# Performance work log

Hardware: AMD Instinct MI355X
Metric: run time of the kernel (lower is better)

Reference implementation:

```python
import jax, jax.numpy as jnp
import numpy as np

N_EMBD = 1024
N_HEAD = 16
B, T = 8, 1024

def setup_inputs() -> dict:
    key = jax.random.key(0)
    ks = jax.random.split(key, 5)
    s = 0.02
    return {
        'x': jax.random.normal(ks[0], (B, T, N_EMBD), dtype=jnp.float32),
        'w_attn': jax.random.normal(ks[1], (N_EMBD, 3 * N_EMBD), dtype=jnp.float32) * s,
        'b_attn': jax.random.normal(ks[2], (3 * N_EMBD,), dtype=jnp.float32) * s,
        'w_proj': jax.random.normal(ks[3], (N_EMBD, N_EMBD), dtype=jnp.float32) * s,
        'b_proj': jax.random.normal(ks[4], (N_EMBD,), dtype=jnp.float32) * s,
    }

def reference(x, w_attn, b_attn, w_proj, b_proj):
    Bb, Tt, C = x.shape
    hd = C // N_HEAD  # head dim
    qkv = x @ w_attn + b_attn                      # [B,T,3C]
    q, k, v = jnp.split(qkv, 3, axis=2)
    # [B,T,C] -> [B,H,T,hd]
    def to_heads(t):
        return t.reshape(Bb, Tt, N_HEAD, hd).transpose(0, 2, 1, 3)
    q, k, v = to_heads(q), to_heads(k), to_heads(v)
    scale = 1.0 / jnp.sqrt(jnp.asarray(hd, dtype=x.dtype))
    att = jnp.einsum('bhqd,bhkd->bhqk', q, k) * scale  # [B,H,T,T]
    causal = jnp.tril(jnp.ones((Tt, Tt), dtype=bool))  # [T,T]
    att = jnp.where(causal[None, None, :, :], att, -jnp.inf)
    att = jax.nn.softmax(att, axis=-1)
    y = jnp.einsum('bhqk,bhkd->bhqd', att, v)          # [B,H,T,hd]
    y = y.transpose(0, 2, 1, 3).reshape(Bb, Tt, C)
    y = y @ w_proj + b_proj
    return y
```

## Files before the change

### kernel.cpp

```cpp
#include <hip/hip_runtime.h>
#include <stdint.h>

#define N_EMBD 1024
#define NHEAD  16
#define HDIM   64
#define BATCH  8
#define SEQ    1024
#define MROWS  (BATCH*SEQ)

typedef __bf16 bf16x8 __attribute__((ext_vector_type(8)));
typedef float  f32x4  __attribute__((ext_vector_type(4)));

__device__ inline unsigned short f2bf(float f) {
  uint32_t u = __float_as_uint(f);
  u += 0x7FFFu + ((u >> 16) & 1u);
  return (unsigned short)(u >> 16);
}

__device__ inline f32x4 mfma_bf16(bf16x8 a, bf16x8 b, f32x4 c) {
  return __builtin_amdgcn_mfma_f32_16x16x32_bf16(a, b, c, 0, 0, 0);
}

__device__ inline void gload_lds16(const unsigned short* g, unsigned short* l) {
  __builtin_amdgcn_global_load_lds(
      (const __attribute__((address_space(1))) void*)g,
      (__attribute__((address_space(3))) void*)l,
      16, 0, 0);
}

#define DSB __builtin_amdgcn_sched_barrier(0)
#define BARRIER __builtin_amdgcn_s_barrier()
#define VMC(n) asm volatile("s_waitcnt vmcnt(" #n ")" ::: "memory")
#define LGKM0 asm volatile("s_waitcnt lgkmcnt(0)" ::: "memory"); DSB

__global__ __launch_bounds__(256) void prep_kernel(
    const float* __restrict__ x, unsigned short* __restrict__ xb,
    const float* __restrict__ wa, unsigned short* __restrict__ oa,
    const float* __restrict__ wp, unsigned short* __restrict__ op) {
  int bid = blockIdx.x;
  int t = threadIdx.x;
  if (bid < 8192) {
    int i = (bid * 256 + t) * 4;
    float4 v = *(const float4*)(x + i);
    ushort4 o;
    o.x = f2bf(v.x); o.y = f2bf(v.y); o.z = f2bf(v.z); o.w = f2bf(v.w);
    *(ushort4*)(xb + i) = o;
    return;
  }
  __shared__ unsigned short tile[64 * 72];
  int idx = bid - 8192;
  int bx = idx & 63;
  int ky = idx >> 6;
  const int K = 1024;
  const float* in; unsigned short* out; int N;
  if (bx < 48) { in = wa; out = oa; N = 3072; }
  else         { in = wp; out = op; N = 1024; bx -= 48; }
  int k0 = ky * 64, n0 = bx * 64;
  {
    int col = (t & 15) * 4;
#pragma unroll
    for (int it = 0; it < 4; ++it) {
      int row = (t >> 4) + it * 16;
      float4 v = *(const float4*)(in + (size_t)(k0 + row) * N + n0 + col);
      ushort4 o;
      o.x = f2bf(v.x); o.y = f2bf(v.y); o.z = f2bf(v.z); o.w = f2bf(v.w);
      *(ushort4*)&tile[row * 72 + col] = o;
    }
  }
  __syncthreads();
  {
    int kcol = (t & 7) * 8;
#pragma unroll
    for (int it = 0; it < 2; ++it) {
      int nrow = (t >> 3) + it * 32;
      alignas(16) unsigned short tmp[8];
#pragma unroll
      for (int j = 0; j < 8; ++j) tmp[j] = tile[(kcol + j) * 72 + nrow];
      *(uint4*)(out + (size_t)(n0 + nrow) * K + k0 + kcol) = *(const uint4*)tmp;
    }
  }
}

__global__ __launch_bounds__(256, 3) void gemm_qkv(
    const unsigned short* __restrict__ A, const unsigned short* __restrict__ Bt,
    const float* __restrict__ bias,
    unsigned short* __restrict__ Qo, unsigned short* __restrict__ Ko,
    unsigned short* __restrict__ VTo) {
  __shared__ unsigned short Asl[256 * 64];
  __shared__ unsigned short Bsl[128 * 64];
  const int bid = blockIdx.x;
  const int xcd = bid & 7;
  const int local = bid >> 3;
  const int nchunk = local >> 5;
  const int rem = local & 31;
  const int m0 = (xcd * 4 + (rem >> 3)) * 256;
  const int n0 = (nchunk * 8 + (rem & 7)) * 128;
  const int tid = threadIdx.x;
  const int l = tid & 63, w = tid >> 6;
  const int wr = w >> 1, wc = w & 1;
  const int g = l >> 4, fr = l & 15;
  f32x4 acc[8][4];
#pragma unroll
  for (int i = 0; i < 8; ++i)
#pragma unroll
    for (int j = 0; j < 4; ++j)
#pragma unroll
      for (int r = 0; r < 4; ++r) acc[i][j][r] = 0.0f;
  const int rr = tid >> 3;
  const int cs = ((tid & 7) * 16) ^ ((rr & 7) << 4);
  const char* srcA[8];
  const char* srcB[4];
#pragma unroll
  for (int c = 0; c < 8; ++c)
    srcA[c] = (const char*)A + (size_t)(m0 + c * 32 + rr) * 2048 + cs;
#pragma unroll
  for (int c = 0; c < 4; ++c)
    srcB[c] = (const char*)Bt + (size_t)(n0 + c * 32 + rr) * 2048 + cs;
  const int ldso = tid * 8;
  const int arow = (wr * 128 + fr) * 128;
  const int brow = (wc * 64 + fr) * 128;
  int colk[2];
  colk[0] = (g * 16) ^ ((fr & 7) << 4);
  colk[1] = (64 + g * 16) ^ ((fr & 7) << 4);
  for (int kt = 0; kt < 16; ++kt) {
    __syncthreads();
#pragma unroll
    for (int c = 0; c < 8; ++c)
      gload_lds16((const unsigned short*)(srcA[c] + kt * 128), &Asl[ldso + c * 2048]);
#pragma unroll
    for (int c = 0; c < 4; ++c)
      gload_lds16((const unsigned short*)(srcB[c] + kt * 128), &Bsl[ldso + c * 2048]);
    __syncthreads();
#pragma unroll
    for (int ks = 0; ks < 2; ++ks) {
      bf16x8 bv[4], av[4];
#pragma unroll
      for (int n = 0; n < 4; ++n)
        bv[n] = *(const bf16x8*)((const char*)Bsl + brow + n * 16 * 128 + colk[ks]);
#pragma unroll
      for (int m = 0; m < 4; ++m)
        av[m] = *(const bf16x8*)((const char*)Asl + arow + m * 16 * 128 + colk[ks]);
#pragma unroll
      for (int n = 0; n < 4; ++n)
#pragma unroll
        for (int m = 0; m < 4; ++m)
          acc[m][n] = mfma_bf16(av[m], bv[n], acc[m][n]);
#pragma unroll
      for (int m = 0; m < 4; ++m)
        av[m] = *(const bf16x8*)((const char*)Asl + arow + (m + 4) * 16 * 128 + colk[ks]);
#pragma unroll
      for (int n = 0; n < 4; ++n)
#pragma unroll
        for (int m = 0; m < 4; ++m)
          acc[m + 4][n] = mfma_bf16(av[m], bv[n], acc[m + 4][n]);
    }
  }
#pragma unroll
  for (int i = 0; i < 8; ++i) {
    int mb = m0 + wr * 128 + i * 16 + 4 * g;
    int bidx = mb >> 10;
    int t = mb & 1023;
#pragma unroll
    for (int j = 0; j < 4; ++j) {
      int n = n0 + wc * 64 + j * 16 + fr;
      float bv2 = bias[n];
      int part = n >> 10;
      int nn2 = n & 1023;
      int h = nn2 >> 6, d = nn2 & 63;
      if (part == 2) {
        alignas(8) unsigned short pk[4];
#pragma unroll
        for (int r = 0; r < 4; ++r) pk[r] = f2bf(acc[i][j][r] + bv2);
        *(ushort4*)&VTo[((size_t)(bidx * NHEAD + h) * HDIM + d) * SEQ + t] =
            *(const ushort4*)pk;
      } else {
        unsigned short* dst = (part == 0) ? Qo : Ko;
        float scl = (part == 0) ? 0.18033688f : 1.0f;
        size_t base = ((size_t)(bidx * NHEAD + h) * SEQ + t) * HDIM + d;
#pragma unroll
        for (int r = 0; r < 4; ++r)
          dst[base + (size_t)r * HDIM] = f2bf((acc[i][j][r] + bv2) * scl);
      }
    }
  }
}

__global__ __launch_bounds__(256) void gemm_proj(
    const unsigned short* __restrict__ A, const unsigned short* __restrict__ Bt,
    const float* __restrict__ bias, float* __restrict__ Out) {
  __shared__ unsigned short Asl[2][8192];
  __shared__ unsigned short Bsl[2][8192];
  const int bid = blockIdx.x;
  const int xcd = bid & 7;
  const int local = bid >> 3;
  const int m0 = (xcd * 8 + (local >> 3)) * 128;
  const int n0 = (local & 7) * 128;
  const int tid = threadIdx.x;
  const int l = tid & 63, w = tid >> 6;
  const int wr = w >> 1, wc = w & 1;
  const int g = l >> 4, fr = l & 15;
  f32x4 acc[4][4];
#pragma unroll
  for (int i = 0; i < 4; ++i)
#pragma unroll
    for (int j = 0; j < 4; ++j)
#pragma unroll
      for (int r = 0; r < 4; ++r) acc[i][j][r] = 0.0f;
  const int rr = tid >> 3;
  const int cs = ((tid & 7) * 16) ^ ((rr & 7) << 4);
  const char* srcA[4]; const char* srcB[4];
#pragma unroll
  for (int c = 0; c < 4; ++c) {
    srcA[c] = (const char*)A + (size_t)(m0 + c * 32 + rr) * 2048 + cs;
    srcB[c] = (const char*)Bt + (size_t)(n0 + c * 32 + rr) * 2048 + cs;
  }
  const int ldso = tid * 8;
  const int arow = (wr * 64 + fr) * 128;
  const int brow = (wc * 64 + fr) * 128;
  int colk[2];
  colk[0] = (g * 16) ^ ((fr & 7) << 4);
  colk[1] = (64 + g * 16) ^ ((fr & 7) << 4);
#pragma unroll
  for (int c = 0; c < 4; ++c)
    gload_lds16((const unsigned short*)(srcA[c]), &Asl[0][ldso + c * 2048]);
#pragma unroll
  for (int c = 0; c < 4; ++c)
    gload_lds16((const unsigned short*)(srcB[c]), &Bsl[0][ldso + c * 2048]);
#pragma unroll
  for (int c = 0; c < 4; ++c)
    gload_lds16((const unsigned short*)(srcA[c] + 128), &Asl[1][ldso + c * 2048]);
#pragma unroll
  for (int c = 0; c < 4; ++c)
    gload_lds16((const unsigned short*)(srcB[c] + 128), &Bsl[1][ldso + c * 2048]);
  for (int kt = 0; kt < 16; ++kt) {
    const int cur = kt & 1;
    if (kt < 15) { VMC(8); } else { VMC(0); }
    DSB; BARRIER; DSB;
#pragma unroll
    for (int ks = 0; ks < 2; ++ks) {
      bf16x8 av[4], bv[4];
#pragma unroll
      for (int m = 0; m < 4; ++m)
        av[m] = *(const bf16x8*)((const char*)&Asl[cur][0] + arow + m * 16 * 128 + colk[ks]);
#pragma unroll
      for (int n = 0; n < 4; ++n)
        bv[n] = *(const bf16x8*)((const char*)&Bsl[cur][0] + brow + n * 16 * 128 + colk[ks]);
#pragma unroll
      for (int n = 0; n < 4; ++n)
#pragma unroll
        for (int m = 0; m < 4; ++m)
          acc[m][n] = mfma_bf16(av[m], bv[n], acc[m][n]);
    }
    LGKM0; BARRIER; DSB;
    if (kt < 14) {
      const int ko = (kt + 2) * 128;
#pragma unroll
      for (int c = 0; c < 4; ++c)
        gload_lds16((const unsigned short*)(srcA[c] + ko), &Asl[cur][ldso + c * 2048]);
#pragma unroll
      for (int c = 0; c < 4; ++c)
        gload_lds16((const unsigned short*)(srcB[c] + ko), &Bsl[cur][ldso + c * 2048]);
    }
  }
#pragma unroll
  for (int i = 0; i < 4; ++i) {
    int mb = m0 + wr * 64 + i * 16 + 4 * g;
#pragma unroll
    for (int j = 0; j < 4; ++j) {
      int n = n0 + wc * 64 + j * 16 + fr;
      float bv2 = bias[n];
#pragma unroll
      for (int r = 0; r < 4; ++r)
        Out[(size_t)(mb + r) * N_EMBD + n] = acc[i][j][r] + bv2;
    }
  }
}

__global__ __launch_bounds__(256) void attn_kernel(
    const unsigned short* __restrict__ Q, const unsigned short* __restrict__ Kv,
    const unsigned short* __restrict__ VT, unsigned short* __restrict__ Y) {
  __shared__ unsigned short Kt[2][4096];
  __shared__ unsigned short Vt[2][4096];
  __shared__ unsigned short p_lds[4 * 32 * 72];
  __shared__ float smx[4][32];
  int tid = threadIdx.x, l = tid & 63, w = tid >> 6;
  int bid = blockIdx.x;
  int swz = (bid & 7) * 64 + (bid >> 3);
  int bh = swz >> 2;
  int pairIdx = swz & 3;
  int b = bh >> 4, h = bh & 15;
  const unsigned short* Qb = Q + (size_t)bh * SEQ * HDIM;
  const char* Kc = (const char*)(Kv + (size_t)bh * SEQ * HDIM);
  const char* Vc = (const char*)(VT + (size_t)bh * HDIM * SEQ);
  unsigned short* pw = &p_lds[w * 32 * 72];
  const int g = l >> 4;
  const int fr = l & 15;

  const int P0 = tid * 16, P1 = tid * 16 + 4096;
  const int r0 = P0 >> 7, r1 = P1 >> 7;
  const int s0 = (P0 & 127) ^ ((r0 & 7) << 4);
  const int s1 = (P1 & 127) ^ ((r1 & 7) << 4);
  const char* Kg0 = Kc + r0 * 128 + s0;
  const char* Kg1 = Kc + r1 * 128 + s1;
  const char* Vg0 = Vc + (size_t)r0 * 2048 + s0;
  const char* Vg1 = Vc + (size_t)r1 * 2048 + s1;

  const int bc = (16 * g) ^ ((l & 7) << 4);

  for (int part = 0; part < 2; ++part) {
    const int qt = (part == 0) ? pairIdx : 7 - pairIdx;
    const int q0 = qt * 128;
    const int wq = q0 + w * 32;

    bf16x8 aq[2][2];
#pragma unroll
    for (int i = 0; i < 2; ++i)
#pragma unroll
      for (int ik = 0; ik < 2; ++ik)
        aq[i][ik] = *(const bf16x8*)&Qb[(size_t)(wq + i * 16 + fr) * HDIM + ik * 32 + 8 * g];

    float mrun[2], lpart[2];
    mrun[0] = mrun[1] = 0.0f;
    lpart[0] = lpart[1] = 0.0f;
    f32x4 acc_o[2][4];
#pragma unroll
    for (int i = 0; i < 2; ++i)
#pragma unroll
      for (int jd = 0; jd < 4; ++jd)
#pragma unroll
        for (int r = 0; r < 4; ++r) acc_o[i][jd][r] = 0.0f;

    const int n_it = (q0 + 128) >> 6;

    gload_lds16((const unsigned short*)(Kg0), &Kt[0][P0 >> 1]);
    gload_lds16((const unsigned short*)(Kg1), &Kt[0][P1 >> 1]);
    gload_lds16((const unsigned short*)(Vg0), &Vt[0][P0 >> 1]);
    gload_lds16((const unsigned short*)(Vg1), &Vt[0][P1 >> 1]);

    for (int it = 0; it < n_it; ++it) {
      const int kv0 = it << 6;
      const int cur = it & 1;
      if (it + 1 < n_it) {
        const int nx = kv0 + 64;
        gload_lds16((const unsigned short*)(Kg0 + nx * 128), &Kt[cur ^ 1][P0 >> 1]);
        gload_lds16((const unsigned short*)(Kg1 + nx * 128), &Kt[cur ^ 1][P1 >> 1]);
        gload_lds16((const unsigned short*)(Vg0 + nx * 2),   &Vt[cur ^ 1][P0 >> 1]);
        gload_lds16((const unsigned short*)(Vg1 + nx * 2),   &Vt[cur ^ 1][P1 >> 1]);
        VMC(4);
      } else {
        VMC(0);
      }
      DSB; BARRIER; DSB;

      const char* Kbuf = (const char*)Kt[cur];
      const char* Vbuf = (const char*)Vt[cur];

      f32x4 s2[2][4];
#pragma unroll
      for (int i = 0; i < 2; ++i)
#pragma unroll
        for (int j = 0; j < 4; ++j)
#pragma unroll
          for (int r = 0; r < 4; ++r) s2[i][j][r] = 0.0f;

      __builtin_amdgcn_s_setprio(1);
#pragma unroll
      for (int ik = 0; ik < 2; ++ik) {
#pragma unroll
        for (int j = 0; j < 4; ++j) {
          bf16x8 bk = *(const bf16x8*)(Kbuf + (j * 16 + fr) * 128 + (bc ^ (ik << 6)));
#pragma unroll
          for (int i = 0; i < 2; ++i) s2[i][j] = mfma_bf16(bk, aq[i][ik], s2[i][j]);
        }
      }
      __builtin_amdgcn_s_setprio(0);

      bool need_mask = (kv0 + 63) > wq;
      if (need_mask) {
#pragma unroll
        for (int i = 0; i < 2; ++i) {
          int q = wq + i * 16 + fr;
#pragma unroll
          for (int j = 0; j < 4; ++j)
#pragma unroll
            for (int r = 0; r < 4; ++r) {
              int kv = kv0 + j * 16 + 4 * g + r;
              if (kv > q) s2[i][j][r] = -3.0e38f;
            }
        }
      }

      float pmloc[2];
#pragma unroll
      for (int i = 0; i < 2; ++i) {
        float m01 = fmaxf(fmaxf(s2[i][0][0], s2[i][0][1]), fmaxf(s2[i][0][2], s2[i][0][3]));
        float m11 = fmaxf(fmaxf(s2[i][1][0], s2[i][1][1]), fmaxf(s2[i][1][2], s2[i][1][3]));
        float m21 = fmaxf(fmaxf(s2[i][2][0], s2[i][2][1]), fmaxf(s2[i][2][2], s2[i][2][3]));
        float m31 = fmaxf(fmaxf(s2[i][3][0], s2[i][3][1]), fmaxf(s2[i][3][2], s2[i][3][3]));
        pmloc[i] = fmaxf(fmaxf(m01, m11), fmaxf(m21, m31));
      }
      bool ok = (pmloc[0] <= mrun[0] + 11.5409f) && (pmloc[1] <= mrun[1] + 11.5409f);
      if (!__all(ok)) {
#pragma unroll
        for (int i = 0; i < 2; ++i) {
          float mm = pmloc[i];
          mm = fmaxf(mm, __shfl_xor(mm, 16, 64));
          mm = fmaxf(mm, __shfl_xor(mm, 32, 64));
          float mn = fmaxf(mrun[i], mm);
          float sc = exp2f(mrun[i] - mn);
          mrun[i] = mn;
          lpart[i] *= sc;
          if (g == 0) smx[w][i * 16 + fr] = sc;
        }
        asm volatile("s_waitcnt lgkmcnt(0)" ::: "memory");
#pragma unroll
        for (int i = 0; i < 2; ++i)
#pragma unroll
          for (int r = 0; r < 4; ++r) {
            float sc = smx[w][i * 16 + 4 * g + r];
#pragma unroll
            for (int jd = 0; jd < 4; ++jd) acc_o[i][jd][r] *= sc;
          }
      }

#pragma unroll
      for (int i = 0; i < 2; ++i) {
#pragma unroll
        for (int j = 0; j < 4; ++j) {
          float p0 = exp2f(s2[i][j][0] - mrun[i]);
          float p1 = exp2f(s2[i][j][1] - mrun[i]);
          float p2 = exp2f(s2[i][j][2] - mrun[i]);
          float p3 = exp2f(s2[i][j][3] - mrun[i]);
          lpart[i] += (p0 + p1) + (p2 + p3);
          uint2 pk2;
          asm("v_cvt_pk_bf16_f32 %0, %1, %2" : "=v"(pk2.x) : "v"(p0), "v"(p1));
          asm("v_cvt_pk_bf16_f32 %0, %1, %2" : "=v"(pk2.y) : "v"(p2), "v"(p3));
          *(uint2*)&pw[(i * 16 + fr) * 72 + j * 16 + 4 * g] = pk2;
        }
      }

      __builtin_amdgcn_s_setprio(1);
#pragma unroll
      for (int ik2 = 0; ik2 < 2; ++ik2) {
        bf16x8 ap[2];
#pragma unroll
        for (int i = 0; i < 2; ++i)
          ap[i] = *(const bf16x8*)&pw[(i * 16 + fr) * 72 + ik2 * 32 + 8 * g];
#pragma unroll
        for (int jd = 0; jd < 4; ++jd) {
          bf16x8 bv = *(const bf16x8*)(Vbuf + (jd * 16 + fr) * 128 + (bc ^ (ik2 << 6)));
#pragma unroll
          for (int i = 0; i < 2; ++i) acc_o[i][jd] = mfma_bf16(ap[i], bv, acc_o[i][jd]);
        }
      }
      __builtin_amdgcn_s_setprio(0);

      asm volatile("s_waitcnt lgkmcnt(0)" ::: "memory");
      DSB; BARRIER; DSB;
    }

#pragma unroll
    for (int i = 0; i < 2; ++i) {
      float t = lpart[i];
      t += __shfl_xor(t, 16, 64);
      t += __shfl_xor(t, 32, 64);
      if (g == 0) smx[w][i * 16 + fr] = t;
    }
    asm volatile("s_waitcnt lgkmcnt(0)" ::: "memory");
#pragma unroll
    for (int i = 0; i < 2; ++i)
#pragma unroll
      for (int r = 0; r < 4; ++r) {
        float inv = 1.0f / smx[w][i * 16 + 4 * g + r];
        int q = wq + i * 16 + 4 * g + r;
#pragma unroll
        for (int jd = 0; jd < 4; ++jd)
          Y[((size_t)b * SEQ + q) * N_EMBD + h * HDIM + jd * 16 + fr] =
              f2bf(acc_o[i][jd][r] * inv);
      }
  }
}

extern "C" void kernel_launch(void* const* d_in, const int* in_sizes, int n_in,
                              void* d_out, int out_size, void* d_ws, size_t ws_size,
                              hipStream_t stream) {
  (void)in_sizes; (void)n_in; (void)out_size; (void)ws_size;
  const float* x      = (const float*)d_in[0];
  const float* w_attn = (const float*)d_in[1];
  const float* b_attn = (const float*)d_in[2];
  const float* w_proj = (const float*)d_in[3];
  const float* b_proj = (const float*)d_in[4];
  float* out = (float*)d_out;

  char* ws = (char*)d_ws;
  size_t off = 0;
  auto carve = [&](size_t bytes) -> char* {
    char* p = ws + off;
    off += (bytes + 255) & ~(size_t)255;
    return p;
  };
  unsigned short* xb     = (unsigned short*)carve((size_t)MROWS * N_EMBD * 2);
  unsigned short* wTattn = (unsigned short*)carve((size_t)3 * N_EMBD * N_EMBD * 2);
  unsigned short* wTproj = (unsigned short*)carve((size_t)N_EMBD * N_EMBD * 2);
  unsigned short* Qb     = (unsigned short*)carve((size_t)MROWS * N_EMBD * 2);
  unsigned short* Kb     = (unsigned short*)carve((size_t)MROWS * N_EMBD * 2);
  unsigned short* VTb    = (unsigned short*)carve((size_t)MROWS * N_EMBD * 2);
  unsigned short* Yb     = (unsigned short*)carve((size_t)MROWS * N_EMBD * 2);
  carve(4096);

  prep_kernel<<<dim3(8192 + 1024), 256, 0, stream>>>(x, xb, w_attn, wTattn, w_proj, wTproj);
  gemm_qkv<<<dim3(768), 256, 0, stream>>>(xb, wTattn, b_attn, Qb, Kb, VTb);
  attn_kernel<<<dim3(512), 256, 0, stream>>>(Qb, Kb, VTb, Yb);
  gemm_proj<<<dim3(512), 256, 0, stream>>>(Yb, wTproj, b_proj, out);
}
```

Measured before the change: 144.9 us.

## Fuse x bf16 cast into QKV GEMM, pipeline it, and stage epilogue through LDS

The separate elementwise cast of x is removed. gemm_qkv now reads fp32 x directly, packs it to bf16 into LDS, and runs a double-buffered 128x128 tile pipeline with register-prefetched A and MFMA under raised priority. The Q/K/V epilogue is staged through LDS so global stores are coalesced 16-byte writes. gemm_proj gets the same load-then-MFMA reordering with setprio. Attention switches from exp2 with a log2e-folded Q scale to __expf with a plain 0.125 scale, which adds a multiply per exponent. The main trade is that x is read as fp32 repeatedly across N tiles instead of once as bf16.

```diff
diff --git a/kernel.cpp b/kernel.cpp
--- a/kernel.cpp
+++ b/kernel.cpp
@@ -33,29 +33,26 @@
 #define VMC(n) asm volatile("s_waitcnt vmcnt(" #n ")" ::: "memory")
 #define LGKM0 asm volatile("s_waitcnt lgkmcnt(0)" ::: "memory"); DSB
 
-__global__ __launch_bounds__(256) void prep_kernel(
-    const float* __restrict__ x, unsigned short* __restrict__ xb,
+__device__ inline uint4 pack8(const f32x4 a, const f32x4 b) {
+  uint4 o;
+  asm("v_cvt_pk_bf16_f32 %0, %1, %2" : "=v"(o.x) : "v"(a[0]), "v"(a[1]));
+  asm("v_cvt_pk_bf16_f32 %0, %1, %2" : "=v"(o.y) : "v"(a[2]), "v"(a[3]));
+  asm("v_cvt_pk_bf16_f32 %0, %1, %2" : "=v"(o.z) : "v"(b[0]), "v"(b[1]));
+  asm("v_cvt_pk_bf16_f32 %0, %1, %2" : "=v"(o.w) : "v"(b[2]), "v"(b[3]));
+  return o;
+}
+
+__global__ __launch_bounds__(256) void transpose_cast2(
     const float* __restrict__ wa, unsigned short* __restrict__ oa,
     const float* __restrict__ wp, unsigned short* __restrict__ op) {
-  int bid = blockIdx.x;
-  int t = threadIdx.x;
-  if (bid < 8192) {
-    int i = (bid * 256 + t) * 4;
-    float4 v = *(const float4*)(x + i);
-    ushort4 o;
-    o.x = f2bf(v.x); o.y = f2bf(v.y); o.z = f2bf(v.z); o.w = f2bf(v.w);
-    *(ushort4*)(xb + i) = o;
-    return;
-  }
   __shared__ unsigned short tile[64 * 72];
-  int idx = bid - 8192;
-  int bx = idx & 63;
-  int ky = idx >> 6;
   const int K = 1024;
+  int bx = blockIdx.x;
   const float* in; unsigned short* out; int N;
   if (bx < 48) { in = wa; out = oa; N = 3072; }
   else         { in = wp; out = op; N = 1024; bx -= 48; }
-  int k0 = ky * 64, n0 = bx * 64;
+  int k0 = blockIdx.y * 64, n0 = bx * 64;
+  int t = threadIdx.x;
   {
     int col = (t & 15) * 4;
 #pragma unroll
@@ -81,106 +78,157 @@
   }
 }
 
-__global__ __launch_bounds__(256, 3) void gemm_qkv(
-    const unsigned short* __restrict__ A, const unsigned short* __restrict__ Bt,
+__global__ __launch_bounds__(256) void gemm_qkv(
+    const float* __restrict__ X, const unsigned short* __restrict__ Bt,
     const float* __restrict__ bias,
     unsigned short* __restrict__ Qo, unsigned short* __restrict__ Ko,
     unsigned short* __restrict__ VTo) {
-  __shared__ unsigned short Asl[256 * 64];
-  __shared__ unsigned short Bsl[128 * 64];
+  __shared__ unsigned short Asl[2][8192];
+  __shared__ unsigned short Bsl[2][8192];
   const int bid = blockIdx.x;
   const int xcd = bid & 7;
   const int local = bid >> 3;
-  const int nchunk = local >> 5;
-  const int rem = local & 31;
-  const int m0 = (xcd * 4 + (rem >> 3)) * 256;
+  const int nchunk = local >> 6;
+  const int rem = local & 63;
+  const int m0 = (xcd * 8 + (rem >> 3)) * 128;
   const int n0 = (nchunk * 8 + (rem & 7)) * 128;
   const int tid = threadIdx.x;
   const int l = tid & 63, w = tid >> 6;
   const int wr = w >> 1, wc = w & 1;
   const int g = l >> 4, fr = l & 15;
-  f32x4 acc[8][4];
-#pragma unroll
-  for (int i = 0; i < 8; ++i)
+  f32x4 acc[4][4];
+#pragma unroll
+  for (int i = 0; i < 4; ++i)
 #pragma unroll
     for (int j = 0; j < 4; ++j)
 #pragma unroll
       for (int r = 0; r < 4; ++r) acc[i][j][r] = 0.0f;
   const int rr = tid >> 3;
   const int cs = ((tid & 7) * 16) ^ ((rr & 7) << 4);
-  const char* srcA[8];
+  const char* srcX[4];
   const char* srcB[4];
 #pragma unroll
-  for (int c = 0; c < 8; ++c)
-    srcA[c] = (const char*)A + (size_t)(m0 + c * 32 + rr) * 2048 + cs;
-#pragma unroll
-  for (int c = 0; c < 4; ++c)
+  for (int c = 0; c < 4; ++c) {
+    srcX[c] = (const char*)X + (size_t)(m0 + c * 32 + rr) * 4096 + 2 * cs;
     srcB[c] = (const char*)Bt + (size_t)(n0 + c * 32 + rr) * 2048 + cs;
+  }
   const int ldso = tid * 8;
-  const int arow = (wr * 128 + fr) * 128;
+  const int arow = (wr * 64 + fr) * 128;
   const int brow = (wc * 64 + fr) * 128;
   int colk[2];
   colk[0] = (g * 16) ^ ((fr & 7) << 4);
   colk[1] = (64 + g * 16) ^ ((fr & 7) << 4);
+
+#pragma unroll
+  for (int c = 0; c < 4; ++c)
+    gload_lds16((const unsigned short*)(srcB[c]), &Bsl[0][ldso + c * 2048]);
+#pragma unroll
+  for (int c = 0; c < 4; ++c)
+    gload_lds16((const unsigned short*)(srcB[c] + 128), &Bsl[1][ldso + c * 2048]);
+#pragma unroll
+  for (int c = 0; c < 4; ++c) {
+    f32x4 a0 = *(const f32x4*)(srcX[c]);
+    f32x4 a1 = *(const f32x4*)(srcX[c] + 16);
+    *(uint4*)&Asl[0][ldso + c * 2048] = pack8(a0, a1);
+    a0 = *(const f32x4*)(srcX[c] + 256);
+    a1 = *(const f32x4*)(srcX[c] + 256 + 16);
+    *(uint4*)&Asl[1][ldso + c * 2048] = pack8(a0, a1);
+  }
+  LGKM0;
+
   for (int kt = 0; kt < 16; ++kt) {
-    __syncthreads();
-#pragma unroll
-    for (int c = 0; c < 8; ++c)
-      gload_lds16((const unsigned short*)(srcA[c] + kt * 128), &Asl[ldso + c * 2048]);
-#pragma unroll
-    for (int c = 0; c < 4; ++c)
-      gload_lds16((const unsigned short*)(srcB[c] + kt * 128), &Bsl[ldso + c * 2048]);
-    __syncthreads();
+    const int cur = kt & 1;
+    if (kt < 15) { VMC(4); } else { VMC(0); }
+    DSB; BARRIER; DSB;
+    f32x4 fa[4][2];
+    if (kt < 14) {
+      const int ko = (kt + 2) * 256;
+#pragma unroll
+      for (int c = 0; c < 4; ++c) {
+        fa[c][0] = *(const f32x4*)(srcX[c] + ko);
+        fa[c][1] = *(const f32x4*)(srcX[c] + ko + 16);
+      }
+    }
+    bf16x8 av[2][4], bv[2][4];
 #pragma unroll
     for (int ks = 0; ks < 2; ++ks) {
-      bf16x8 bv[4], av[4];
+#pragma unroll
+      for (int m = 0; m < 4; ++m)
+        av[ks][m] = *(const bf16x8*)((const char*)&Asl[cur][0] + arow +
+                                     m * 16 * 128 + colk[ks]);
 #pragma unroll
       for (int n = 0; n < 4; ++n)
-        bv[n] = *(const bf16x8*)((const char*)Bsl + brow + n * 16 * 128 + colk[ks]);
-#pragma unroll
-      for (int m = 0; m < 4; ++m)
-        av[m] = *(const bf16x8*)((const char*)Asl + arow + m * 16 * 128 + colk[ks]);
+        bv[ks][n] = *(const bf16x8*)((const char*)&Bsl[cur][0] + brow +
+                                     n * 16 * 128 + colk[ks]);
+    }
+    LGKM0; BARRIER; DSB;
+    if (kt < 14) {
+      const int ko = (kt + 2) * 128;
+#pragma unroll
+      for (int c = 0; c < 4; ++c)
+        *(uint4*)&Asl[cur][ldso + c * 2048] = pack8(fa[c][0], fa[c][1]);
+#pragma unroll
+      for (int c = 0; c < 4; ++c)
+        gload_lds16((const unsigned short*)(srcB[c] + ko),
+                    &Bsl[cur][ldso + c * 2048]);
+    }
+    __builtin_amdgcn_s_setprio(1);
+#pragma unroll
+    for (int ks = 0; ks < 2; ++ks)
 #pragma unroll
       for (int n = 0; n < 4; ++n)
 #pragma unroll
         for (int m = 0; m < 4; ++m)
-          acc[m][n] = mfma_bf16(av[m], bv[n], acc[m][n]);
-#pragma unroll
-      for (int m = 0; m < 4; ++m)
-        av[m] = *(const bf16x8*)((const char*)Asl + arow + (m + 4) * 16 * 128 + colk[ks]);
-#pragma unroll
-      for (int n = 0; n < 4; ++n)
-#pragma unroll
-        for (int m = 0; m < 4; ++m)
-          acc[m + 4][n] = mfma_bf16(av[m], bv[n], acc[m + 4][n]);
-    }
-  }
-#pragma unroll
-  for (int i = 0; i < 8; ++i) {
-    int mb = m0 + wr * 128 + i * 16 + 4 * g;
-    int bidx = mb >> 10;
-    int t = mb & 1023;
-#pragma unroll
-    for (int j = 0; j < 4; ++j) {
-      int n = n0 + wc * 64 + j * 16 + fr;
-      float bv2 = bias[n];
-      int part = n >> 10;
-      int nn2 = n & 1023;
-      int h = nn2 >> 6, d = nn2 & 63;
-      if (part == 2) {
-        alignas(8) unsigned short pk[4];
-#pragma unroll
-        for (int r = 0; r < 4; ++r) pk[r] = f2bf(acc[i][j][r] + bv2);
-        *(ushort4*)&VTo[((size_t)(bidx * NHEAD + h) * HDIM + d) * SEQ + t] =
-            *(const ushort4*)pk;
-      } else {
-        unsigned short* dst = (part == 0) ? Qo : Ko;
-        float scl = (part == 0) ? 0.18033688f : 1.0f;
-        size_t base = ((size_t)(bidx * NHEAD + h) * SEQ + t) * HDIM + d;
+          acc[m][n] = mfma_bf16(av[ks][m], bv[ks][n], acc[m][n]);
+    __builtin_amdgcn_s_setprio(0);
+  }
+
+  const int nw0 = n0 + wc * 64;
+  const int part = nw0 >> 10;
+  const int h = (nw0 & 1023) >> 6;
+  const int mw0 = m0 + wr * 64;
+  const int bidx = mw0 >> 10;
+  const int t0 = mw0 & 1023;
+  unsigned short* stg = (w < 3) ? ((unsigned short*)Asl + w * 4608)
+                                : ((unsigned short*)Bsl);
+  float bvj[4];
+#pragma unroll
+  for (int j = 0; j < 4; ++j) bvj[j] = bias[nw0 + j * 16 + fr];
+  if (part < 2) {
+    const float scl = (part == 0) ? 0.125f : 1.0f;
+#pragma unroll
+    for (int i = 0; i < 4; ++i)
+#pragma unroll
+      for (int j = 0; j < 4; ++j)
 #pragma unroll
         for (int r = 0; r < 4; ++r)
-          dst[base + (size_t)r * HDIM] = f2bf((acc[i][j][r] + bv2) * scl);
-      }
+          stg[(i * 16 + 4 * g + r) * 72 + j * 16 + fr] =
+              f2bf((acc[i][j][r] + bvj[j]) * scl);
+    LGKM0;
+    unsigned short* dst = (part == 0) ? Qo : Ko;
+    size_t base = ((size_t)(bidx * NHEAD + h) * SEQ + t0) * HDIM + (l & 7) * 8;
+#pragma unroll
+    for (int it = 0; it < 8; ++it) {
+      int row = (l >> 3) + it * 8;
+      uint4 v = *(const uint4*)&stg[row * 72 + (l & 7) * 8];
+      *(uint4*)&dst[base + (size_t)row * HDIM] = v;
+    }
+  } else {
+#pragma unroll
+    for (int i = 0; i < 4; ++i)
+#pragma unroll
+      for (int j = 0; j < 4; ++j)
+#pragma unroll
+        for (int r = 0; r < 4; ++r)
+          stg[(j * 16 + fr) * 72 + i * 16 + 4 * g + r] =
+              f2bf(acc[i][j][r] + bvj[j]);
+    LGKM0;
+    size_t base = ((size_t)(bidx * NHEAD + h) * HDIM) * SEQ + t0 + (l & 7) * 8;
+#pragma unroll
+    for (int it = 0; it < 8; ++it) {
+      int row = (l >> 3) + it * 8;
+      uint4 v = *(const uint4*)&stg[row * 72 + (l & 7) * 8];
+      *(uint4*)&VTo[base + (size_t)row * SEQ] = v;
     }
   }
 }
@@ -236,20 +284,17 @@
     const int cur = kt & 1;
     if (kt < 15) { VMC(8); } else { VMC(0); }
     DSB; BARRIER; DSB;
+    bf16x8 av[2][4], bv[2][4];
 #pragma unroll
     for (int ks = 0; ks < 2; ++ks) {
-      bf16x8 av[4], bv[4];
 #pragma unroll
       for (int m = 0; m < 4; ++m)
-        av[m] = *(const bf16x8*)((const char*)&Asl[cur][0] + arow + m * 16 * 128 + colk[ks]);
+        av[ks][m] = *(const bf16x8*)((const char*)&Asl[cur][0] + arow +
+                                     m * 16 * 128 + colk[ks]);
 #pragma unroll
       for (int n = 0; n < 4; ++n)
-        bv[n] = *(const bf16x8*)((const char*)&Bsl[cur][0] + brow + n * 16 * 128 + colk[ks]);
-#pragma unroll
-      for (int n = 0; n < 4; ++n)
-#pragma unroll
-        for (int m = 0; m < 4; ++m)
-          acc[m][n] = mfma_bf16(av[m], bv[n], acc[m][n]);
+        bv[ks][n] = *(const bf16x8*)((const char*)&Bsl[cur][0] + brow +
+                                     n * 16 * 128 + colk[ks]);
     }
     LGKM0; BARRIER; DSB;
     if (kt < 14) {
@@ -261,6 +306,15 @@
       for (int c = 0; c < 4; ++c)
         gload_lds16((const unsigned short*)(srcB[c] + ko), &Bsl[cur][ldso + c * 2048]);
     }
+    __builtin_amdgcn_s_setprio(1);
+#pragma unroll
+    for (int ks = 0; ks < 2; ++ks)
+#pragma unroll
+      for (int n = 0; n < 4; ++n)
+#pragma unroll
+        for (int m = 0; m < 4; ++m)
+          acc[m][n] = mfma_bf16(av[ks][m], bv[ks][n], acc[m][n]);
+    __builtin_amdgcn_s_setprio(0);
   }
 #pragma unroll
   for (int i = 0; i < 4; ++i) {
@@ -399,7 +453,7 @@
         float m31 = fmaxf(fmaxf(s2[i][3][0], s2[i][3][1]), fmaxf(s2[i][3][2], s2[i][3][3]));
         pmloc[i] = fmaxf(fmaxf(m01, m11), fmaxf(m21, m31));
       }
-      bool ok = (pmloc[0] <= mrun[0] + 11.5409f) && (pmloc[1] <= mrun[1] + 11.5409f);
+      bool ok = (pmloc[0] <= mrun[0] + 8.0f) && (pmloc[1] <= mrun[1] + 8.0f);
       if (!__all(ok)) {
 #pragma unroll
         for (int i = 0; i < 2; ++i) {
@@ -407,7 +461,7 @@
           mm = fmaxf(mm, __shfl_xor(mm, 16, 64));
           mm = fmaxf(mm, __shfl_xor(mm, 32, 64));
           float mn = fmaxf(mrun[i], mm);
-          float sc = exp2f(mrun[i] - mn);
+          float sc = __expf(mrun[i] - mn);
           mrun[i] = mn;
           lpart[i] *= sc;
           if (g == 0) smx[w][i * 16 + fr] = sc;
@@ -427,10 +481,10 @@
       for (int i = 0; i < 2; ++i) {
 #pragma unroll
         for (int j = 0; j < 4; ++j) {
-          float p0 = exp2f(s2[i][j][0] - mrun[i]);
-          float p1 = exp2f(s2[i][j][1] - mrun[i]);
-          float p2 = exp2f(s2[i][j][2] - mrun[i]);
-          float p3 = exp2f(s2[i][j][3] - mrun[i]);
+          float p0 = __expf(s2[i][j][0] - mrun[i]);
+          float p1 = __expf(s2[i][j][1] - mrun[i]);
+          float p2 = __expf(s2[i][j][2] - mrun[i]);
+          float p3 = __expf(s2[i][j][3] - mrun[i]);
           lpart[i] += (p0 + p1) + (p2 + p3);
           uint2 pk2;
           asm("v_cvt_pk_bf16_f32 %0, %1, %2" : "=v"(pk2.x) : "v"(p0), "v"(p1));
@@ -499,7 +553,6 @@
     off += (bytes + 255) & ~(size_t)255;
     return p;
   };
-  unsigned short* xb     = (unsigned short*)carve((size_t)MROWS * N_EMBD * 2);
   unsigned short* wTattn = (unsigned short*)carve((size_t)3 * N_EMBD * N_EMBD * 2);
   unsigned short* wTproj = (unsigned short*)carve((size_t)N_EMBD * N_EMBD * 2);
   unsigned short* Qb     = (unsigned short*)carve((size_t)MROWS * N_EMBD * 2);
@@ -508,8 +561,8 @@
   unsigned short* Yb     = (unsigned short*)carve((size_t)MROWS * N_EMBD * 2);
   carve(4096);
 
-  prep_kernel<<<dim3(8192 + 1024), 256, 0, stream>>>(x, xb, w_attn, wTattn, w_proj, wTproj);
-  gemm_qkv<<<dim3(768), 256, 0, stream>>>(xb, wTattn, b_attn, Qb, Kb, VTb);
+  transpose_cast2<<<dim3(64, 16), 256, 0, stream>>>(w_attn, wTattn, w_proj, wTproj);
+  gemm_qkv<<<dim3(1536), 256, 0, stream>>>(x, wTattn, b_attn, Qb, Kb, VTb);
   attn_kernel<<<dim3(512), 256, 0, stream>>>(Qb, Kb, VTb, Yb);
   gemm_proj<<<dim3(512), 256, 0, stream>>>(Yb, wTproj, b_proj, out);
 }
```

New measurement: 146.3 us. No clear change (+1.0%).
